# Performance work log

Hardware: AMD Instinct MI355X
Metric: run time of the kernel (lower is better)

## Reference

```python
import jax, jax.numpy as jnp
import numpy as np

D_MODEL, N_HEADS, D_K, D_V = 1024, 16, 64, 64


def setup_inputs() -> dict:
    key = jax.random.key(0)
    ks = jax.random.split(key, 9)
    B, S = 8, 1024
    Q = jax.random.normal(ks[0], (B, S, D_MODEL), dtype=jnp.float32)
    K = jax.random.normal(ks[1], (B, S, D_MODEL), dtype=jnp.float32)
    V = jax.random.normal(ks[2], (B, S, D_MODEL), dtype=jnp.float32)
    # Xavier-uniform weights (gain=1): limit = sqrt(6/(fan_in+fan_out))
    lim = float(np.sqrt(6.0 / (D_MODEL + N_HEADS * D_K)))
    Wq = jax.random.uniform(ks[3], (D_MODEL, N_HEADS * D_K), minval=-lim, maxval=lim, dtype=jnp.float32)
    Wk = jax.random.uniform(ks[4], (D_MODEL, N_HEADS * D_K), minval=-lim, maxval=lim, dtype=jnp.float32)
    Wv = jax.random.uniform(ks[5], (D_MODEL, N_HEADS * D_V), minval=-lim, maxval=lim, dtype=jnp.float32)
    # nn.Linear default bias init: uniform(-1/sqrt(fan_in), 1/sqrt(fan_in))
    bl = float(1.0 / np.sqrt(D_MODEL))
    bq = jax.random.uniform(ks[6], (N_HEADS * D_K,), minval=-bl, maxval=bl, dtype=jnp.float32)
    bk = jax.random.uniform(ks[7], (N_HEADS * D_K,), minval=-bl, maxval=bl, dtype=jnp.float32)
    bv = jax.random.uniform(ks[8], (N_HEADS * D_V,), minval=-bl, maxval=bl, dtype=jnp.float32)
    return {"Q": Q, "K": K, "V": V, "Wq": Wq, "bq": bq, "Wk": Wk, "bk": bk, "Wv": Wv, "bv": bv}


def reference(Q, K, V, Wq, bq, Wk, bk, Wv, bv):
    B, S, _ = Q.shape
    # projections -> [B, H, S, d]
    q = (Q @ Wq + bq).reshape(B, S, N_HEADS, D_K).transpose(0, 2, 1, 3)
    k = (K @ Wk + bk).reshape(B, S, N_HEADS, D_K).transpose(0, 2, 1, 3)
    v = (V @ Wv + bv).reshape(B, S, N_HEADS, D_V).transpose(0, 2, 1, 3)
    scores = jnp.exp(jnp.einsum('bhqd,bhkd->bhqk', q, k) / jnp.sqrt(jnp.float32(D_K)))
    attn = scores / (jnp.sum(scores, axis=-1, keepdims=True) + 1e-8)
    ctx = jnp.einsum('bhqk,bhkd->bhqd', attn, v)  # [B,H,S,Dv]
    return ctx.transpose(0, 2, 1, 3).reshape(B, S, N_HEADS * D_V)
```

## Files before the change

### kernel.cpp

```cpp
#include <hip/hip_runtime.h>
#include <stdint.h>

#define DM 1024
#define HEADS 16
#define BATCH 8
#define SEQ 1024
#define MTOT 8192

typedef _Float16 half8 __attribute__((ext_vector_type(8)));
typedef _Float16 half4 __attribute__((ext_vector_type(4)));
typedef float floatx4 __attribute__((ext_vector_type(4)));

__device__ __forceinline__ void glds16(const void* g, void* l) {
    __builtin_amdgcn_global_load_lds(
        (const __attribute__((address_space(1))) void*)g,
        (__attribute__((address_space(3))) void*)l, 16, 0, 0);
}

__global__ __launch_bounds__(256) void cvt_inputs(
        const float* __restrict__ Q, const float* __restrict__ K,
        const float* __restrict__ V,
        _Float16* __restrict__ qb, _Float16* __restrict__ kb, _Float16* __restrict__ vb) {
    const float* src = blockIdx.y == 0 ? Q : (blockIdx.y == 1 ? K : V);
    _Float16* dst    = blockIdx.y == 0 ? qb : (blockIdx.y == 1 ? kb : vb);
    size_t i = ((size_t)blockIdx.x * 256 + threadIdx.x) * 8;
    float4 a = *(const float4*)(src + i);
    float4 b = *(const float4*)(src + i + 4);
    half8 h;
    h[0] = (_Float16)a.x; h[1] = (_Float16)a.y; h[2] = (_Float16)a.z; h[3] = (_Float16)a.w;
    h[4] = (_Float16)b.x; h[5] = (_Float16)b.y; h[6] = (_Float16)b.z; h[7] = (_Float16)b.w;
    *(half8*)(dst + i) = h;
}

__global__ __launch_bounds__(256) void cvt_w(
        const float* __restrict__ Wq, const float* __restrict__ Wk,
        const float* __restrict__ Wv,
        _Float16* __restrict__ wqt, _Float16* __restrict__ wkt, _Float16* __restrict__ wvt) {
    __shared__ float t[32][33];
    int z = blockIdx.z;
    const float* W = z == 0 ? Wq : (z == 1 ? Wk : Wv);
    _Float16* Wt   = z == 0 ? wqt : (z == 1 ? wkt : wvt);
    int k0 = blockIdx.x * 32, n0 = blockIdx.y * 32;
    int tx = threadIdx.x, ty = threadIdx.y;
#pragma unroll
    for (int i = 0; i < 4; i++)
        t[ty + i * 8][tx] = W[(size_t)(k0 + ty + i * 8) * DM + n0 + tx];
    __syncthreads();
#pragma unroll
    for (int i = 0; i < 4; i++)
        Wt[(size_t)(n0 + ty + i * 8) * DM + k0 + tx] = (_Float16)t[tx][ty + i * 8];
}

__global__ __launch_bounds__(256) void proj_gemm(
        const _Float16* __restrict__ qb, const _Float16* __restrict__ kb,
        const _Float16* __restrict__ vb,
        const _Float16* __restrict__ wqt, const _Float16* __restrict__ wkt,
        const _Float16* __restrict__ wvt,
        const float* __restrict__ bq, const float* __restrict__ bk,
        const float* __restrict__ bv,
        _Float16* __restrict__ qh, _Float16* __restrict__ kh, _Float16* __restrict__ vT) {
    __shared__ _Float16 As[128 * 64];
    __shared__ _Float16 Bs[128 * 64];
    int z = blockIdx.z;
    const _Float16* A  = z == 0 ? qb : (z == 1 ? kb : vb);
    const _Float16* Bw = z == 0 ? wqt : (z == 1 ? wkt : wvt);
    const float* bias  = z == 0 ? bq : (z == 1 ? bk : bv);
    int m0 = blockIdx.x * 128, n0 = blockIdx.y * 128;
    int tid = threadIdx.x, wid = tid >> 6, lane = tid & 63;
    int l15 = lane & 15, quad = lane >> 4;
    int wm = wid >> 1, wn = wid & 1;
    bool swapped = (z < 2);

    floatx4 acc[4][4] = {};

    for (int kb_ = 0; kb_ < 16; kb_++) {
        __syncthreads();
        int k0 = kb_ * 64;
        int r = (wid * 4) * 8 + (lane >> 3);
        int pg = (lane & 7) ^ (lane >> 3);
#pragma unroll
        for (int ii = 0; ii < 4; ii++) {
            int issue = wid * 4 + ii;
            int rr = r + ii * 8;
            glds16(A  + (size_t)(m0 + rr) * DM + k0 + pg * 8, &As[issue * 512]);
            glds16(Bw + (size_t)(n0 + rr) * DM + k0 + pg * 8, &Bs[issue * 512]);
        }
        __syncthreads();
#pragma unroll
        for (int kc = 0; kc < 2; kc++) {
            half8 a[4], b[4];
#pragma unroll
            for (int mt = 0; mt < 4; mt++) {
                int row = wm * 64 + mt * 16 + l15;
                int pl = (kc * 4 + quad) ^ (l15 & 7);
                a[mt] = *(const half8*)&As[row * 64 + pl * 8];
            }
#pragma unroll
            for (int nt = 0; nt < 4; nt++) {
                int row = wn * 64 + nt * 16 + l15;
                int pl = (kc * 4 + quad) ^ (l15 & 7);
                b[nt] = *(const half8*)&Bs[row * 64 + pl * 8];
            }
            if (swapped) {
#pragma unroll
                for (int mt = 0; mt < 4; mt++)
#pragma unroll
                    for (int nt = 0; nt < 4; nt++)
                        acc[mt][nt] = __builtin_amdgcn_mfma_f32_16x16x32_f16(
                            b[nt], a[mt], acc[mt][nt], 0, 0, 0);
            } else {
#pragma unroll
                for (int mt = 0; mt < 4; mt++)
#pragma unroll
                    for (int nt = 0; nt < 4; nt++)
                        acc[mt][nt] = __builtin_amdgcn_mfma_f32_16x16x32_f16(
                            a[mt], b[nt], acc[mt][nt], 0, 0, 0);
            }
        }
    }

    if (swapped) {
        float sc = (z == 0) ? 0.125f : 1.0f;
        _Float16* out = (z == 0) ? qh : kh;
#pragma unroll
        for (int nt = 0; nt < 4; nt++) {
            int d0 = n0 + wn * 64 + nt * 16 + quad * 4;
            int hh = d0 >> 6, dd = d0 & 63;
            floatx4 b4 = *(const floatx4*)&bias[d0];
#pragma unroll
            for (int mt = 0; mt < 4; mt++) {
                int s = m0 + wm * 64 + mt * 16 + l15;
                int b_ = s >> 10, ss = s & 1023;
                size_t off = ((size_t)(b_ * HEADS + hh)) * 65536 + (size_t)ss * 64 + dd;
                half4 hv;
#pragma unroll
                for (int r = 0; r < 4; r++)
                    hv[r] = (_Float16)((acc[mt][nt][r] + b4[r]) * sc);
                *(half4*)&out[off] = hv;
            }
        }
    } else {
#pragma unroll
        for (int nt = 0; nt < 4; nt++) {
            int d = n0 + wn * 64 + nt * 16 + l15;
            int hh = d >> 6, dd = d & 63;
            float bv_ = bias[d];
#pragma unroll
            for (int mt = 0; mt < 4; mt++) {
                int s0 = m0 + wm * 64 + mt * 16 + quad * 4;
                int b_ = s0 >> 10, ss = s0 & 1023;
                size_t off = ((size_t)(b_ * HEADS + hh)) * 65536 + (size_t)dd * 1024 + ss;
                half4 hv;
#pragma unroll
                for (int r = 0; r < 4; r++)
                    hv[r] = (_Float16)(acc[mt][nt][r] + bv_);
                *(half4*)&vT[off] = hv;
            }
        }
    }
}

__global__ __launch_bounds__(256) void attn(
        const _Float16* __restrict__ qh, const _Float16* __restrict__ kh,
        const _Float16* __restrict__ vT, float* __restrict__ out) {
    __shared__ _Float16 Ks[4096];
    __shared__ _Float16 Vs[4096];
    __shared__ _Float16 QP[16384];
    int qt = blockIdx.x, h = blockIdx.y, b = blockIdx.z;
    size_t base = ((size_t)(b * HEADS + h)) * 65536;
    int tid = threadIdx.x, wid = tid >> 6, lane = tid & 63;
    int l15 = lane & 15, quad = lane >> 4;
    int rs = lane >> 3;
    int pg = (lane & 7) ^ rs;

#pragma unroll
    for (int ii = 0; ii < 8; ii++) {
        int issue = wid * 8 + ii;
        int r = issue * 8 + rs;
        glds16(qh + base + (size_t)(qt * 256 + r) * 64 + pg * 8, &QP[issue * 512]);
    }
    __syncthreads();
    half8 qf[4][2];
#pragma unroll
    for (int mt = 0; mt < 4; mt++)
#pragma unroll
        for (int kc = 0; kc < 2; kc++) {
            int row = wid * 64 + mt * 16 + l15;
            int pl = (kc * 4 + quad) ^ (l15 & 7);
            qf[mt][kc] = *(const half8*)&QP[row * 64 + pl * 8];
        }
    __syncthreads();

    floatx4 oacc[4][4] = {};
    float rden[4] = {0.f, 0.f, 0.f, 0.f};
    _Float16* Pw = &QP[wid * 4096];

    for (int kt = 0; kt < 16; kt++) {
        __syncthreads();
#pragma unroll
        for (int ii = 0; ii < 2; ii++) {
            int issue = wid * 2 + ii;
            int r = issue * 8 + rs;
            glds16(kh + base + (size_t)(kt * 64 + r) * 64 + pg * 8, &Ks[issue * 512]);
            glds16(vT + base + (size_t)r * 1024 + kt * 64 + pg * 8, &Vs[issue * 512]);
        }
        __syncthreads();

#pragma unroll
        for (int hf = 0; hf < 2; hf++) {
            floatx4 sacc[2][4] = {};
#pragma unroll
            for (int kc = 0; kc < 2; kc++) {
                half8 kf[2];
#pragma unroll
                for (int kn2 = 0; kn2 < 2; kn2++) {
                    int kn = hf * 2 + kn2;
                    int pl = (kc * 4 + quad) ^ (l15 & 7);
                    kf[kn2] = *(const half8*)&Ks[(kn * 16 + l15) * 64 + pl * 8];
                }
#pragma unroll
                for (int kn2 = 0; kn2 < 2; kn2++)
#pragma unroll
                    for (int mt = 0; mt < 4; mt++)
                        sacc[kn2][mt] = __builtin_amdgcn_mfma_f32_16x16x32_f16(
                            kf[kn2], qf[mt][kc], sacc[kn2][mt], 0, 0, 0);
            }
#pragma unroll
            for (int kn2 = 0; kn2 < 2; kn2++) {
                int kn = hf * 2 + kn2;
#pragma unroll
                for (int mt = 0; mt < 4; mt++) {
                    half4 ph;
#pragma unroll
                    for (int r = 0; r < 4; r++) {
                        float p = __expf(sacc[kn2][mt][r]);
                        rden[mt] += p;
                        ph[r] = (_Float16)p;
                    }
                    *(half4*)&Pw[(kn * 2 + (quad >> 1)) * 512 + (mt * 16 + l15) * 8 +
                                 (quad & 1) * 4] = ph;
                }
            }
            half8 af[4], vf[4];
#pragma unroll
            for (int mt = 0; mt < 4; mt++)
                af[mt] = *(const half8*)&Pw[(hf * 4 + quad) * 512 + (mt * 16 + l15) * 8];
#pragma unroll
            for (int dn = 0; dn < 4; dn++) {
                int pl = (hf * 4 + quad) ^ (l15 & 7);
                vf[dn] = *(const half8*)&Vs[(dn * 16 + l15) * 64 + pl * 8];
            }
#pragma unroll
            for (int mt = 0; mt < 4; mt++)
#pragma unroll
                for (int dn = 0; dn < 4; dn++)
                    oacc[mt][dn] = __builtin_amdgcn_mfma_f32_16x16x32_f16(
                        af[mt], vf[dn], oacc[mt][dn], 0, 0, 0);
        }
    }

#pragma unroll
    for (int mt = 0; mt < 4; mt++) {
        float d = rden[mt];
        d += __shfl_xor(d, 16, 64);
        d += __shfl_xor(d, 32, 64);
        rden[mt] = 1.0f / (d + 1e-8f);
    }
#pragma unroll
    for (int mt = 0; mt < 4; mt++) {
#pragma unroll
        for (int r = 0; r < 4; r++) {
            float dinv = __shfl(rden[mt], quad * 4 + r, 16);
            int s = qt * 256 + wid * 64 + mt * 16 + quad * 4 + r;
#pragma unroll
            for (int dn = 0; dn < 4; dn++) {
                int col = h * 64 + dn * 16 + l15;
                out[((size_t)(b * SEQ + s)) * 1024 + col] = oacc[mt][dn][r] * dinv;
            }
        }
    }
}

extern "C" void kernel_launch(void* const* d_in, const int* in_sizes, int n_in,
                              void* d_out, int out_size, void* d_ws, size_t ws_size,
                              hipStream_t stream) {
    const float* Q  = (const float*)d_in[0];
    const float* K  = (const float*)d_in[1];
    const float* V  = (const float*)d_in[2];
    const float* Wq = (const float*)d_in[3];
    const float* bq = (const float*)d_in[4];
    const float* Wk = (const float*)d_in[5];
    const float* bk = (const float*)d_in[6];
    const float* Wv = (const float*)d_in[7];
    const float* bv = (const float*)d_in[8];
    float* out = (float*)d_out;

    char* ws = (char*)d_ws;
    const size_t TEN = (size_t)MTOT * DM * sizeof(_Float16);
    _Float16* qb  = (_Float16*)(ws);
    _Float16* kb  = (_Float16*)(ws + TEN);
    _Float16* vb  = (_Float16*)(ws + 2 * TEN);
    _Float16* qh  = (_Float16*)(ws + 3 * TEN);
    _Float16* kh  = (_Float16*)(ws + 4 * TEN);
    _Float16* vT  = (_Float16*)(ws + 5 * TEN);
    const size_t WTN = (size_t)DM * DM * sizeof(_Float16);
    _Float16* wqt = (_Float16*)(ws + 6 * TEN);
    _Float16* wkt = (_Float16*)(ws + 6 * TEN + WTN);
    _Float16* wvt = (_Float16*)(ws + 6 * TEN + 2 * WTN);

    cvt_inputs<<<dim3(4096, 3), 256, 0, stream>>>(Q, K, V, qb, kb, vb);
    cvt_w<<<dim3(32, 32, 3), dim3(32, 8), 0, stream>>>(Wq, Wk, Wv, wqt, wkt, wvt);
    proj_gemm<<<dim3(64, 8, 3), 256, 0, stream>>>(qb, kb, vb, wqt, wkt, wvt,
                                                  bq, bk, bv, qh, kh, vT);
    attn<<<dim3(4, 16, 8), 256, 0, stream>>>(qh, kh, vT, out);
}
```

Baseline: 281.3 us.

## Load projection GEMM operands directly from global memory, dropping LDS staging

The projection GEMM no longer stages A and B tiles through shared memory with async global-to-LDS loads and barriers. Each wave now reads its MFMA fragments straight from global memory in 32-wide K steps, and the swapped and unswapped paths become separate loops. This removes the barriers and LDS traffic, but cross-wave reuse now depends on the L1/L2 caches and the loads are strided 16-byte reads with no explicit prefetch.

Result: slower. 390.3 us (+38.7%).

```diff
diff --git a/kernel.cpp b/kernel.cpp
--- a/kernel.cpp
+++ b/kernel.cpp
@@ -59,8 +59,6 @@
         const float* __restrict__ bq, const float* __restrict__ bk,
         const float* __restrict__ bv,
         _Float16* __restrict__ qh, _Float16* __restrict__ kh, _Float16* __restrict__ vT) {
-    __shared__ _Float16 As[128 * 64];
-    __shared__ _Float16 Bs[128 * 64];
     int z = blockIdx.z;
     const _Float16* A  = z == 0 ? qb : (z == 1 ? kb : vb);
     const _Float16* Bw = z == 0 ? wqt : (z == 1 ? wkt : wvt);
@@ -71,51 +69,42 @@
     int wm = wid >> 1, wn = wid & 1;
     bool swapped = (z < 2);
 
+    const _Float16* Ab = A  + (size_t)(m0 + wm * 64 + l15) * DM + quad * 8;
+    const _Float16* Bb = Bw + (size_t)(n0 + wn * 64 + l15) * DM + quad * 8;
+
     floatx4 acc[4][4] = {};
 
-    for (int kb_ = 0; kb_ < 16; kb_++) {
-        __syncthreads();
-        int k0 = kb_ * 64;
-        int r = (wid * 4) * 8 + (lane >> 3);
-        int pg = (lane & 7) ^ (lane >> 3);
-#pragma unroll
-        for (int ii = 0; ii < 4; ii++) {
-            int issue = wid * 4 + ii;
-            int rr = r + ii * 8;
-            glds16(A  + (size_t)(m0 + rr) * DM + k0 + pg * 8, &As[issue * 512]);
-            glds16(Bw + (size_t)(n0 + rr) * DM + k0 + pg * 8, &Bs[issue * 512]);
-        }
-        __syncthreads();
-#pragma unroll
-        for (int kc = 0; kc < 2; kc++) {
+    if (swapped) {
+        for (int k0 = 0; k0 < DM; k0 += 32) {
             half8 a[4], b[4];
 #pragma unroll
-            for (int mt = 0; mt < 4; mt++) {
-                int row = wm * 64 + mt * 16 + l15;
-                int pl = (kc * 4 + quad) ^ (l15 & 7);
-                a[mt] = *(const half8*)&As[row * 64 + pl * 8];
-            }
-#pragma unroll
-            for (int nt = 0; nt < 4; nt++) {
-                int row = wn * 64 + nt * 16 + l15;
-                int pl = (kc * 4 + quad) ^ (l15 & 7);
-                b[nt] = *(const half8*)&Bs[row * 64 + pl * 8];
-            }
-            if (swapped) {
-#pragma unroll
-                for (int mt = 0; mt < 4; mt++)
-#pragma unroll
-                    for (int nt = 0; nt < 4; nt++)
-                        acc[mt][nt] = __builtin_amdgcn_mfma_f32_16x16x32_f16(
-                            b[nt], a[mt], acc[mt][nt], 0, 0, 0);
-            } else {
-#pragma unroll
-                for (int mt = 0; mt < 4; mt++)
-#pragma unroll
-                    for (int nt = 0; nt < 4; nt++)
-                        acc[mt][nt] = __builtin_amdgcn_mfma_f32_16x16x32_f16(
-                            a[mt], b[nt], acc[mt][nt], 0, 0, 0);
-            }
+            for (int mt = 0; mt < 4; mt++)
+                a[mt] = *(const half8*)(Ab + (size_t)mt * 16 * DM + k0);
+#pragma unroll
+            for (int nt = 0; nt < 4; nt++)
+                b[nt] = *(const half8*)(Bb + (size_t)nt * 16 * DM + k0);
+#pragma unroll
+            for (int mt = 0; mt < 4; mt++)
+#pragma unroll
+                for (int nt = 0; nt < 4; nt++)
+                    acc[mt][nt] = __builtin_amdgcn_mfma_f32_16x16x32_f16(
+                        b[nt], a[mt], acc[mt][nt], 0, 0, 0);
+        }
+    } else {
+        for (int k0 = 0; k0 < DM; k0 += 32) {
+            half8 a[4], b[4];
+#pragma unroll
+            for (int mt = 0; mt < 4; mt++)
+                a[mt] = *(const half8*)(Ab + (size_t)mt * 16 * DM + k0);
+#pragma unroll
+            for (int nt = 0; nt < 4; nt++)
+                b[nt] = *(const half8*)(Bb + (size_t)nt * 16 * DM + k0);
+#pragma unroll
+            for (int mt = 0; mt < 4; mt++)
+#pragma unroll
+                for (int nt = 0; nt < 4; nt++)
+                    acc[mt][nt] = __builtin_amdgcn_mfma_f32_16x16x32_f16(
+                        a[mt], b[nt], acc[mt][nt], 0, 0, 0);
         }
     }
 
```
